# Optimization experiments

Measured on AMD Instinct MI355X. Metric: run time of the kernel, lower is better.

Reference implementation:

```python
import jax, jax.numpy as jnp
import numpy as np

N = 100000      # nodes
E = 600000      # directed edges
D_IN = 128
D_H = 128
D_OUT = 128
EPS = 1e-5      # BatchNorm eps


def setup_inputs() -> dict:
    key = jax.random.key(0)
    ks = jax.random.split(key, 6)
    x = jax.random.normal(ks[0], (N, D_IN), dtype=jnp.float32)
    edge_index = jax.random.randint(ks[1], (2, E), 0, N, dtype=jnp.int64)
    s1 = 1.0 / np.sqrt(D_IN)
    s2 = 1.0 / np.sqrt(D_H)
    W1 = jax.random.uniform(ks[2], (D_IN, D_H), minval=-s1, maxval=s1, dtype=jnp.float32)
    b1 = jnp.zeros((D_H,), jnp.float32)
    gamma1 = jnp.ones((D_H,), jnp.float32)
    beta1 = jnp.zeros((D_H,), jnp.float32)
    W2 = jax.random.uniform(ks[3], (D_H, D_OUT), minval=-s2, maxval=s2, dtype=jnp.float32)
    b2 = jnp.zeros((D_OUT,), jnp.float32)
    return dict(x=x, edge_index=edge_index, W1=W1, b1=b1,
                gamma1=gamma1, beta1=beta1, W2=W2, b2=b2)


def _gcn_conv(x, W, b, src, dst):
    # PyG GCNConv: h = D^{-1/2} (A + I) D^{-1/2} (x @ W) + b
    n = x.shape[0]
    h = x @ W                                   # [N, d_out]
    loop = jnp.arange(n, dtype=src.dtype)
    s = jnp.concatenate([src, loop])            # self loops appended
    d = jnp.concatenate([dst, loop])
    deg = jax.ops.segment_sum(jnp.ones_like(d, jnp.float32), d, num_segments=n)
    dinv = jax.lax.rsqrt(deg)                   # deg >= 1 after self loops
    norm = dinv[s] * dinv[d]                    # [E + N]
    agg = jax.ops.segment_sum(h[s] * norm[:, None], d, num_segments=n)  # [N, d_out]
    return agg + b


def reference(x, edge_index, W1, b1, gamma1, beta1, W2, b2):
    src, dst = edge_index[0], edge_index[1]
    # layer 0: GCNConv -> BatchNorm1d (training batch stats) -> ReLU (dropout p=0)
    h = _gcn_conv(x, W1, b1, src, dst)
    mean = h.mean(axis=0)
    var = h.var(axis=0)                         # biased variance, as torch BN
    h = (h - mean) * jax.lax.rsqrt(var + EPS) * gamma1 + beta1
    h = jax.nn.relu(h)
    # final layer: GCNConv only
    return _gcn_conv(h, W2, b2, src, dst)
```

## Files before the change

kernel.cpp:

```cpp
#include <hip/hip_runtime.h>

#define D 128
#define EPSV 1e-5f

typedef __attribute__((ext_vector_type(8))) short bf16x8;
typedef __attribute__((ext_vector_type(4))) float f32x4;

__device__ __forceinline__ short f2bf(float f){
  unsigned u = __float_as_uint(f);
  u += 0x7fffu + ((u >> 16) & 1u);
  return (short)(u >> 16);
}
__device__ __forceinline__ float bflo(unsigned u){ return __uint_as_float(u << 16); }
__device__ __forceinline__ float bfhi(unsigned u){ return __uint_as_float(u & 0xffff0000u); }
__device__ __forceinline__ float bf2f(short s){ return __uint_as_float(((unsigned)(unsigned short)s) << 16); }
__device__ __forceinline__ unsigned packbf(float a, float b){
  unsigned lo = (unsigned short)f2bf(a);
  unsigned hi = (unsigned short)f2bf(b);
  return lo | (hi << 16);
}

__global__ void k_init(int N, int E, const int* __restrict__ ei, int* __restrict__ flag,
                       int* __restrict__ deg, int* __restrict__ fill, float* __restrict__ gpart,
                       const float* __restrict__ W1, const float* __restrict__ W2,
                       short* __restrict__ w1t, short* __restrict__ w2t){
  int i = blockIdx.x*blockDim.x + threadIdx.x;
  if (i < N){ deg[i] = 0; fill[i] = 0; }
  if (i < D*D){
    int j = i >> 7, k = i & 127;
    w1t[i] = f2bf(W1[k*D + j]);
    w2t[i] = f2bf(W2[k*D + j]);
  }
  if (i < 2048) gpart[i] = 0.f;
  if (blockIdx.x == 0){
    __shared__ int any;
    int t = threadIdx.x;
    if (t == 0) any = 0;
    __syncthreads();
    if (2*t+1 < 2*E && ei[2*t+1] != 0) atomicOr(&any, 1);
    __syncthreads();
    if (t == 0) flag[0] = (any == 0) ? 1 : 0;
  }
}

__global__ void k_count(const int* __restrict__ ei, int E, const int* __restrict__ flag,
                        int* __restrict__ deg){
  int e = blockIdx.x*blockDim.x + threadIdx.x;
  if (e >= E) return;
  int d = flag[0] ? ei[2*E + 2*e] : ei[E + e];
  atomicAdd(&deg[d], 1);
}

__global__ void k_dinv_bsum(const int* __restrict__ deg, int N, float* __restrict__ dinv,
                            int* __restrict__ bsum){
  __shared__ int sh[256];
  int t = threadIdx.x, base = blockIdx.x*1024;
  int s = 0;
  for (int i = t; i < 1024; i += 256){
    int j = base + i;
    if (j < N){ int dg = deg[j]; dinv[j] = rsqrtf((float)(dg + 1)); s += dg; }
  }
  sh[t] = s; __syncthreads();
  for (int d = 128; d > 0; d >>= 1){ if (t < d) sh[t] += sh[t+d]; __syncthreads(); }
  if (t == 0) bsum[blockIdx.x] = sh[0];
}

__global__ void k_scan_bsum(int NB, const int* __restrict__ bsum, int* __restrict__ boff){
  __shared__ int sh[128];
  int t = threadIdx.x;
  int v = (t < NB) ? bsum[t] : 0;
  sh[t] = v; __syncthreads();
  for (int d = 1; d < 128; d <<= 1){
    int u = (t >= d) ? sh[t-d] : 0;
    __syncthreads();
    sh[t] += u;
    __syncthreads();
  }
  if (t < NB) boff[t] = sh[t] - v;
}

__global__ void k_rowptr(const int* __restrict__ deg, int N, const int* __restrict__ boff,
                         int* __restrict__ row_ptr){
  __shared__ int sh[256];
  int t = threadIdx.x;
  int base = blockIdx.x*1024 + t*4;
  int c0 = (base+0 < N) ? deg[base+0] : 0;
  int c1 = (base+1 < N) ? deg[base+1] : 0;
  int c2 = (base+2 < N) ? deg[base+2] : 0;
  int c3 = (base+3 < N) ? deg[base+3] : 0;
  int s = c0 + c1 + c2 + c3;
  sh[t] = s; __syncthreads();
  for (int d = 1; d < 256; d <<= 1){
    int v = (t >= d) ? sh[t-d] : 0;
    __syncthreads();
    sh[t] += v;
    __syncthreads();
  }
  int o = sh[t] - s + boff[blockIdx.x];
  if (base+0 < N) row_ptr[base+0] = o; o += c0;
  if (base+1 < N) row_ptr[base+1] = o; o += c1;
  if (base+2 < N) row_ptr[base+2] = o; o += c2;
  if (base+3 < N) row_ptr[base+3] = o;
}

__global__ void k_scatter(const int* __restrict__ ei, int E, const int* __restrict__ flag,
                          const int* __restrict__ rowp, int* __restrict__ fill,
                          const float* __restrict__ dinv, int2* __restrict__ epack){
  int e = blockIdx.x*blockDim.x + threadIdx.x;
  if (e >= E) return;
  int s, d;
  if (flag[0]){ s = ei[2*e]; d = ei[2*E + 2*e]; }
  else        { s = ei[e];   d = ei[E + e];     }
  int pos = rowp[d] + atomicAdd(&fill[d], 1);
  int2 ev; ev.x = s; ev.y = __float_as_int(dinv[s] * dinv[d]);
  epack[pos] = ev;
}

template<int MODE>
__global__ __launch_bounds__(256, 2) void k_gemm(const void* __restrict__ A,
                                const short* __restrict__ BT, short* __restrict__ C, int N,
                                const float* __restrict__ scale, const float* __restrict__ shift){
  int lane = threadIdx.x & 63;
  int m = lane & 15, quad = lane >> 4;
  bf16x8 b[4][8];
  #pragma unroll
  for (int kc = 0; kc < 4; ++kc)
    #pragma unroll
    for (int c = 0; c < 8; ++c)
      b[kc][c] = *(const bf16x8*)(BT + (c*16 + m)*D + kc*32 + quad*8);

  int tiles = (N + 31) >> 5;
  int wid = blockIdx.x*4 + (threadIdx.x >> 6);
  int wstride = gridDim.x*4;
  for (int tile = wid; tile < tiles; tile += wstride){
    int r0 = tile << 5;
    bf16x8 a[2][4];
    #pragma unroll
    for (int g = 0; g < 2; ++g){
      int row = r0 + g*16 + m;
      if (row >= N) row = N - 1;
      #pragma unroll
      for (int kc = 0; kc < 4; ++kc){
        int k0 = kc*32 + quad*8;
        if (MODE == 1){
          const float* Af = (const float*)A + (size_t)row*D + k0;
          float4 u = *(const float4*)Af;
          float4 v = *(const float4*)(Af + 4);
          bf16x8 tv;
          tv[0]=f2bf(u.x); tv[1]=f2bf(u.y); tv[2]=f2bf(u.z); tv[3]=f2bf(u.w);
          tv[4]=f2bf(v.x); tv[5]=f2bf(v.y); tv[6]=f2bf(v.z); tv[7]=f2bf(v.w);
          a[g][kc] = tv;
        } else if (MODE == 2){
          bf16x8 raw = *(const bf16x8*)((const short*)A + (size_t)row*D + k0);
          float4 s0v = *(const float4*)(scale + k0);
          float4 s1v = *(const float4*)(scale + k0 + 4);
          float4 h0v = *(const float4*)(shift + k0);
          float4 h1v = *(const float4*)(shift + k0 + 4);
          bf16x8 tv;
          tv[0] = f2bf(fmaxf(fmaf(bf2f(raw[0]), s0v.x, h0v.x), 0.f));
          tv[1] = f2bf(fmaxf(fmaf(bf2f(raw[1]), s0v.y, h0v.y), 0.f));
          tv[2] = f2bf(fmaxf(fmaf(bf2f(raw[2]), s0v.z, h0v.z), 0.f));
          tv[3] = f2bf(fmaxf(fmaf(bf2f(raw[3]), s0v.w, h0v.w), 0.f));
          tv[4] = f2bf(fmaxf(fmaf(bf2f(raw[4]), s1v.x, h1v.x), 0.f));
          tv[5] = f2bf(fmaxf(fmaf(bf2f(raw[5]), s1v.y, h1v.y), 0.f));
          tv[6] = f2bf(fmaxf(fmaf(bf2f(raw[6]), s1v.z, h1v.z), 0.f));
          tv[7] = f2bf(fmaxf(fmaf(bf2f(raw[7]), s1v.w, h1v.w), 0.f));
          a[g][kc] = tv;
        } else {
          a[g][kc] = *(const bf16x8*)((const short*)A + (size_t)row*D + k0);
        }
      }
    }
    f32x4 acc[2][8];
    #pragma unroll
    for (int g = 0; g < 2; ++g)
      #pragma unroll
      for (int c = 0; c < 8; ++c) acc[g][c] = (f32x4){0.f,0.f,0.f,0.f};
    #pragma unroll
    for (int kc = 0; kc < 4; ++kc)
      #pragma unroll
      for (int g = 0; g < 2; ++g)
        #pragma unroll
        for (int c = 0; c < 8; ++c)
          acc[g][c] = __builtin_amdgcn_mfma_f32_16x16x32_bf16(a[g][kc], b[kc][c], acc[g][c], 0, 0, 0);
    #pragma unroll
    for (int g = 0; g < 2; ++g)
      #pragma unroll
      for (int c = 0; c < 8; ++c)
        #pragma unroll
        for (int r = 0; r < 4; ++r){
          int rr = r0 + g*16 + quad*4 + r;
          if (rr < N) C[(size_t)rr*D + c*16 + m] = f2bf(acc[g][c][r]);
        }
  }
}

template<int OUTF32>
__global__ __launch_bounds__(256) void k_agg(const short* __restrict__ H, const int* __restrict__ rowp,
        const int* __restrict__ deg, const int2* __restrict__ epack, const float* __restrict__ dinv,
        const float* __restrict__ bias, void* __restrict__ out, int N, float* __restrict__ gpart){
  int w = threadIdx.x >> 6, p = threadIdx.x & 63;
  int wid = blockIdx.x*4 + w, wstride = gridDim.x*4;
  const unsigned* Hu = (const unsigned*)H;
  float S0=0.f, S1=0.f, Q0=0.f, Q1=0.f;
  for (int n = wid; n < N; n += wstride){
    float d1 = dinv[n], w0 = d1*d1;
    unsigned u = Hu[(size_t)n*64 + p];
    float a0 = w0 * bflo(u), a1 = w0 * bfhi(u);
    int start = rowp[n], cnt = deg[n];
    for (int base = 0; base < cnt; base += 64){
      int nb = cnt - base; if (nb > 64) nb = 64;
      int2 ev;
      if (p < nb) ev = epack[start + base + p];
      else { ev.x = 0; ev.y = 0; }
      for (int j = 0; j < nb; j += 8){
        int s0 = __shfl(ev.x, j+0), s1 = __shfl(ev.x, j+1);
        int s2 = __shfl(ev.x, j+2), s3 = __shfl(ev.x, j+3);
        int s4 = __shfl(ev.x, j+4), s5 = __shfl(ev.x, j+5);
        int s6 = __shfl(ev.x, j+6), s7 = __shfl(ev.x, j+7);
        float f0 = __int_as_float(__shfl(ev.y, j+0));
        float f1 = __int_as_float(__shfl(ev.y, j+1));
        float f2 = __int_as_float(__shfl(ev.y, j+2));
        float f3 = __int_as_float(__shfl(ev.y, j+3));
        float f4 = __int_as_float(__shfl(ev.y, j+4));
        float f5 = __int_as_float(__shfl(ev.y, j+5));
        float f6 = __int_as_float(__shfl(ev.y, j+6));
        float f7 = __int_as_float(__shfl(ev.y, j+7));
        unsigned u0 = Hu[(size_t)s0*64 + p], u1 = Hu[(size_t)s1*64 + p];
        unsigned u2 = Hu[(size_t)s2*64 + p], u3 = Hu[(size_t)s3*64 + p];
        unsigned u4 = Hu[(size_t)s4*64 + p], u5 = Hu[(size_t)s5*64 + p];
        unsigned u6 = Hu[(size_t)s6*64 + p], u7 = Hu[(size_t)s7*64 + p];
        a0 = fmaf(f0, bflo(u0), a0); a1 = fmaf(f0, bfhi(u0), a1);
        a0 = fmaf(f1, bflo(u1), a0); a1 = fmaf(f1, bfhi(u1), a1);
        a0 = fmaf(f2, bflo(u2), a0); a1 = fmaf(f2, bfhi(u2), a1);
        a0 = fmaf(f3, bflo(u3), a0); a1 = fmaf(f3, bfhi(u3), a1);
        a0 = fmaf(f4, bflo(u4), a0); a1 = fmaf(f4, bfhi(u4), a1);
        a0 = fmaf(f5, bflo(u5), a0); a1 = fmaf(f5, bfhi(u5), a1);
        a0 = fmaf(f6, bflo(u6), a0); a1 = fmaf(f6, bfhi(u6), a1);
        a0 = fmaf(f7, bflo(u7), a0); a1 = fmaf(f7, bfhi(u7), a1);
      }
    }
    if (OUTF32){
      float2 r; r.x = a0 + bias[2*p]; r.y = a1 + bias[2*p+1];
      ((float2*)out)[(size_t)n*64 + p] = r;
    } else {
      ((unsigned*)out)[(size_t)n*64 + p] = packbf(a0, a1);
      S0 += a0; Q0 += a0*a0; S1 += a1; Q1 += a1*a1;
    }
  }
  if (!OUTF32){
    __shared__ float ls[1024];
    int base = w*256;
    ls[base + 2*p]       = S0;
    ls[base + 2*p + 1]   = S1;
    ls[base + 128 + 2*p]     = Q0;
    ls[base + 128 + 2*p + 1] = Q1;
    __syncthreads();
    int t = threadIdx.x;
    float v = ls[t] + ls[256 + t] + ls[512 + t] + ls[768 + t];
    atomicAdd(&gpart[(blockIdx.x & 7)*256 + t], v);
  }
}

__global__ void k_ss(const float* __restrict__ gpart, const float* __restrict__ gamma,
                     const float* __restrict__ beta, int N,
                     float* __restrict__ scale, float* __restrict__ shift){
  int f = threadIdx.x;
  if (f < 128){
    float s = 0.f, q = 0.f;
    for (int i = 0; i < 8; ++i){ s += gpart[i*256 + f]; q += gpart[i*256 + 128 + f]; }
    float inv = 1.f / (float)N;
    float mean = s * inv;
    float var  = q * inv - mean*mean;
    float sc = gamma[f] * rsqrtf(var + EPSV);
    scale[f] = sc;
    shift[f] = beta[f] - mean * sc;
  }
}

extern "C" void kernel_launch(void* const* d_in, const int* in_sizes, int n_in,
                              void* d_out, int out_size, void* d_ws, size_t ws_size,
                              hipStream_t stream){
  const float* x   = (const float*)d_in[0];
  const int*   ei  = (const int*)  d_in[1];
  const float* W1  = (const float*)d_in[2];
  const float* g1  = (const float*)d_in[4];
  const float* be1 = (const float*)d_in[5];
  const float* W2  = (const float*)d_in[6];
  const float* b2  = (const float*)d_in[7];
  float* out = (float*)d_out;
  int N = in_sizes[0] / D;
  int E = in_sizes[1] / 2;

  char* w = (char*)d_ws;
  auto carve = [&](size_t bytes)->char*{ char* p = w; w += (bytes + 255) & ~(size_t)255; return p; };
  int*   flag  = (int*)  carve(256);
  int*   degA  = (int*)  carve((size_t)N*4);
  int*   fillA = (int*)  carve((size_t)N*4);
  float* dinvA = (float*)carve((size_t)N*4);
  int*   rowp  = (int*)  carve((size_t)N*4);
  int*   bsum  = (int*)  carve(4096);
  int*   boff  = (int*)  carve(4096);
  int2*  epack = (int2*) carve((size_t)E*8);
  float* gpart = (float*)carve(2048*4);
  float* scale = (float*)carve(512);
  float* shift = (float*)carve(512);
  short* w1t   = (short*)carve((size_t)D*D*2);
  short* w2t   = (short*)carve((size_t)D*D*2);
  short* h1    = (short*)carve((size_t)N*D*2);
  short* hb    = (short*)carve((size_t)N*D*2);

  const int TB = 256;
  int EB  = (E + TB - 1) / TB;
  int NBt = (N + TB - 1) / TB;
  int NB1024 = (N + 1023) / 1024;
  int GEMMB = 512;
  int AGGB  = 2048;

  k_init      <<<NBt, TB, 0, stream>>>(N, E, ei, flag, degA, fillA, gpart, W1, W2, w1t, w2t);
  k_count     <<<EB, TB, 0, stream>>>(ei, E, flag, degA);
  k_dinv_bsum <<<NB1024, 256, 0, stream>>>(degA, N, dinvA, bsum);
  k_scan_bsum <<<1, 128, 0, stream>>>(NB1024, bsum, boff);
  k_rowptr    <<<NB1024, 256, 0, stream>>>(degA, N, boff, rowp);
  k_scatter   <<<EB, TB, 0, stream>>>(ei, E, flag, rowp, fillA, dinvA, epack);
  k_gemm<1>   <<<GEMMB, 256, 0, stream>>>(x, w1t, h1, N, nullptr, nullptr);
  k_agg<0>    <<<AGGB, 256, 0, stream>>>(h1, rowp, degA, epack, dinvA, nullptr, hb, N, gpart);
  k_ss        <<<1, 128, 0, stream>>>(gpart, g1, be1, N, scale, shift);
  k_gemm<2>   <<<GEMMB, 256, 0, stream>>>(hb, w2t, h1, N, scale, shift);
  k_agg<1>    <<<AGGB, 256, 0, stream>>>(h1, rowp, degA, epack, dinvA, b2, out, N, nullptr);
}
```

Before: 302.0 us.

## Stage GEMM weights in swizzled LDS and coalesce output stores via LDS

The GEMM kernel now loads the transposed weight matrix into an XOR-swizzled LDS buffer instead of holding 32 bf16x8 registers per lane. It also swaps the MFMA operands so each lane's accumulator covers consecutive output columns, then writes results through a per-wave LDS tile so each row is stored with 16-byte vector writes instead of scattered 2-byte writes. This is meant to cut register pressure and make global stores coalesced, at the cost of extra LDS traffic and waits. The unused plain-bf16 GEMM mode is folded into the BN/ReLU path, and the final aggregation now receives gpart instead of null, which looks harmless but is inconsistent.

```diff
diff --git a/kernel.cpp b/kernel.cpp
--- a/kernel.cpp
+++ b/kernel.cpp
@@ -120,17 +120,26 @@
 __global__ __launch_bounds__(256, 2) void k_gemm(const void* __restrict__ A,
                                 const short* __restrict__ BT, short* __restrict__ C, int N,
                                 const float* __restrict__ scale, const float* __restrict__ shift){
+  __shared__ short ldsB[16384];
+  __shared__ short ldsC[4*2048];
+  int w = threadIdx.x >> 6;
   int lane = threadIdx.x & 63;
   int m = lane & 15, quad = lane >> 4;
-  bf16x8 b[4][8];
-  #pragma unroll
-  for (int kc = 0; kc < 4; ++kc)
-    #pragma unroll
-    for (int c = 0; c < 8; ++c)
-      b[kc][c] = *(const bf16x8*)(BT + (c*16 + m)*D + kc*32 + quad*8);
+
+  {
+    const bf16x8* BTv = (const bf16x8*)BT;
+    bf16x8* Bw = (bf16x8*)ldsB;
+    for (int g = threadIdx.x; g < 2048; g += 256){
+      int row = g >> 4, ch = g & 15;
+      Bw[row*16 + (ch ^ (row & 15))] = BTv[g];
+    }
+  }
+  __syncthreads();
+  const bf16x8* Bv = (const bf16x8*)ldsB;
+  short* cw = ldsC + w*2048;
 
   int tiles = (N + 31) >> 5;
-  int wid = blockIdx.x*4 + (threadIdx.x >> 6);
+  int wid = blockIdx.x*4 + w;
   int wstride = gridDim.x*4;
   for (int tile = wid; tile < tiles; tile += wstride){
     int r0 = tile << 5;
@@ -150,7 +159,7 @@
           tv[0]=f2bf(u.x); tv[1]=f2bf(u.y); tv[2]=f2bf(u.z); tv[3]=f2bf(u.w);
           tv[4]=f2bf(v.x); tv[5]=f2bf(v.y); tv[6]=f2bf(v.z); tv[7]=f2bf(v.w);
           a[g][kc] = tv;
-        } else if (MODE == 2){
+        } else {
           bf16x8 raw = *(const bf16x8*)((const short*)A + (size_t)row*D + k0);
           float4 s0v = *(const float4*)(scale + k0);
           float4 s1v = *(const float4*)(scale + k0 + 4);
@@ -166,8 +175,6 @@
           tv[6] = f2bf(fmaxf(fmaf(bf2f(raw[6]), s1v.z, h1v.z), 0.f));
           tv[7] = f2bf(fmaxf(fmaf(bf2f(raw[7]), s1v.w, h1v.w), 0.f));
           a[g][kc] = tv;
-        } else {
-          a[g][kc] = *(const bf16x8*)((const short*)A + (size_t)row*D + k0);
         }
       }
     }
@@ -177,21 +184,37 @@
       #pragma unroll
       for (int c = 0; c < 8; ++c) acc[g][c] = (f32x4){0.f,0.f,0.f,0.f};
     #pragma unroll
-    for (int kc = 0; kc < 4; ++kc)
+    for (int kc = 0; kc < 4; ++kc){
+      bf16x8 bb[8];
+      #pragma unroll
+      for (int c = 0; c < 8; ++c)
+        bb[c] = Bv[(c*16 + m)*16 + ((kc*4 + quad) ^ m)];
       #pragma unroll
       for (int g = 0; g < 2; ++g)
         #pragma unroll
         for (int c = 0; c < 8; ++c)
-          acc[g][c] = __builtin_amdgcn_mfma_f32_16x16x32_bf16(a[g][kc], b[kc][c], acc[g][c], 0, 0, 0);
+          acc[g][c] = __builtin_amdgcn_mfma_f32_16x16x32_bf16(bb[c], a[g][kc], acc[g][c], 0, 0, 0);
+    }
     #pragma unroll
-    for (int g = 0; g < 2; ++g)
-      #pragma unroll
-      for (int c = 0; c < 8; ++c)
-        #pragma unroll
-        for (int r = 0; r < 4; ++r){
-          int rr = r0 + g*16 + quad*4 + r;
-          if (rr < N) C[(size_t)rr*D + c*16 + m] = f2bf(acc[g][c][r]);
-        }
+    for (int g = 0; g < 2; ++g){
+      #pragma unroll
+      for (int c = 0; c < 8; ++c){
+        uint2 v;
+        v.x = packbf(acc[g][c][0], acc[g][c][1]);
+        v.y = packbf(acc[g][c][2], acc[g][c][3]);
+        int x = c*2 + (quad >> 1);
+        *(uint2*)&cw[m*128 + ((x ^ m) << 3) + ((quad & 1) << 2)] = v;
+      }
+      asm volatile("s_waitcnt lgkmcnt(0)" ::: "memory");
+      #pragma unroll
+      for (int rg = 0; rg < 4; ++rg){
+        int lrow = rg*4 + quad;
+        int rr = r0 + g*16 + lrow;
+        uint4 v = *(const uint4*)&cw[lrow*128 + ((m ^ lrow) << 3)];
+        if (rr < N) *(uint4*)(C + (size_t)rr*D + m*8) = v;
+      }
+      asm volatile("s_waitcnt lgkmcnt(0)" ::: "memory");
+    }
   }
 }
 
@@ -327,5 +350,5 @@
   k_agg<0>    <<<AGGB, 256, 0, stream>>>(h1, rowp, degA, epack, dinvA, nullptr, hb, N, gpart);
   k_ss        <<<1, 128, 0, stream>>>(gpart, g1, be1, N, scale, shift);
   k_gemm<2>   <<<GEMMB, 256, 0, stream>>>(hb, w2t, h1, N, scale, shift);
-  k_agg<1>    <<<AGGB, 256, 0, stream>>>(h1, rowp, degA, epack, dinvA, b2, out, N, nullptr);
-}
+  k_agg<1>    <<<AGGB, 256, 0, stream>>>(h1, rowp, degA, epack, dinvA, b2, out, N, gpart);
+}
```

Measured after the change: 266.1 us. 11.9% less time.
